# Kernel optimization log

Hardware: AMD Instinct MI355X
Metric: run time of the kernel (lower is better)

The kernel has to match this reference:

```python
import jax, jax.numpy as jnp
import numpy as np

L, N, E, D, H, B = 4, 50000, 800000, 128, 64, 16384
ED = 2 * D  # edge_dim
K = 7      # conv1d kernel size


def setup_inputs() -> dict:
    key = jax.random.key(0)
    ks = jax.random.split(key, 12)
    return {
        "x_nodes": jax.random.normal(ks[0], (L, N, 1), jnp.float32),
        "edge_index": jax.random.randint(ks[1], (L, 2, E), 0, N),
        "W1": jax.random.normal(ks[2], (L, 1, H), jnp.float32) * 0.1,
        "b1": jnp.zeros((L, H), jnp.float32),
        "gamma": jnp.ones((L, H), jnp.float32),
        "beta": jnp.zeros((L, H), jnp.float32),
        "W2": jax.random.normal(ks[3], (L, H, D), jnp.float32) * 0.05,
        "b2": jnp.zeros((L, D), jnp.float32),
        "conv_w": jax.random.normal(ks[4], (ED, ED, K), jnp.float32) * 0.02,
        "conv_b": jnp.zeros((ED,), jnp.float32),
        "lc_w": jax.random.normal(ks[5], (ED, L), jnp.float32) * 0.05,
        "lc_b": jnp.zeros((L,), jnp.float32),
        "link_w": jax.random.normal(ks[6], (ED, 2), jnp.float32) * 0.05,
        "link_b": jnp.zeros((2,), jnp.float32),
        "now_layer": jax.random.randint(ks[7], (B,), 0, L),
        "leftnode": jax.random.randint(ks[8], (B,), 0, N),
        "rightnode": jax.random.randint(ks[9], (B,), 0, N),
    }


def gcn_conv(x, src, dst, norm, W, b):
    # x: [N, Fin] -> [N, Fout]; symmetric-normalized message passing (GCNConv)
    xw = x @ W
    out = jax.ops.segment_sum(norm[:, None] * xw[src], dst, num_segments=N)
    return out + b


def gcn_layer(x, ei, W1, b1, g, bt, W2, b2):
    loops = jnp.arange(N, dtype=ei.dtype)
    src = jnp.concatenate([ei[0], loops])
    dst = jnp.concatenate([ei[1], loops])
    deg = jax.ops.segment_sum(jnp.ones_like(src, jnp.float32), dst, num_segments=N)
    dis = jax.lax.rsqrt(jnp.maximum(deg, 1e-12))
    norm = dis[src] * dis[dst]
    h = gcn_conv(x, src, dst, norm, W1, b1)
    # BatchNorm1d (training mode: batch stats over nodes)
    mu = h.mean(axis=0)
    var = h.var(axis=0)
    h = g * (h - mu) * jax.lax.rsqrt(var + 1e-5) + bt
    h = jax.nn.relu(h)
    return gcn_conv(h, src, dst, norm, W2, b2)


def reference(x_nodes, edge_index, W1, b1, gamma, beta, W2, b2,
              conv_w, conv_b, lc_w, lc_b, link_w, link_b,
              now_layer, leftnode, rightnode):
    # Per-layer GCN embeddings (fixed small L -> Python loop is fine, keeps peak memory low)
    embeds = jnp.stack([
        gcn_layer(x_nodes[i], edge_index[i], W1[i], b1[i], gamma[i], beta[i], W2[i], b2[i])
        for i in range(L)
    ])  # [L, N, D]

    # Edge features: gather per-sample layer-specific node embeddings and concat
    left = embeds[now_layer, leftnode]    # [B, D]
    right = embeds[now_layer, rightnode]  # [B, D]
    layer_specific = jnp.concatenate([left, right], axis=-1)  # [B, ED]

    # Conv1d applied unbatched on [ED, B] (convolves across batch dim, as in original)
    dn = jax.lax.conv_dimension_numbers((1, ED, B), (ED, ED, K), ('NCH', 'OIH', 'NCH'))
    y = jax.lax.conv_general_dilated(layer_specific.T[None], conv_w, (1,), [(3, 3)],
                                     dimension_numbers=dn)[0]  # [ED, B]
    shared = jax.nn.relu(y + conv_b[:, None]).T  # [B, ED]

    discriminant_outs = shared @ lc_w + lc_b  # [B, L]

    # Ortho_algorithm: remove shared component from specific, combine with shared
    dot = jnp.sum(layer_specific * shared, axis=-1, keepdims=True)
    nrm = jnp.sum(shared * shared, axis=-1, keepdims=True)
    enhanced = layer_specific - (dot / (nrm + 1e-12)) * shared + shared  # [B, ED]

    prediction_outs = enhanced @ link_w + link_b  # [B, 2]
    return prediction_outs, discriminant_outs
```

## Files before the change

### kernel.cpp

```cpp
#include <hip/hip_runtime.h>
#include <hip/hip_bf16.h>

#define Lc 4
#define Nc 50000
#define Ec 800000
#define Bc 16384
#define EDc 256
#define Kc 7
#define Mtot (Lc * Nc)
#define NBK 196
#define KDIM (EDc * Kc)

#define BINW 512
#define FB 98
#define NBINS (FB * Lc)
#define CAPc 12288
#define CHUNK 8192

typedef __attribute__((ext_vector_type(8))) short bf16x8;
typedef __attribute__((ext_vector_type(4))) float f32x4;

static __device__ __forceinline__ unsigned short f2bf(float f) {
    unsigned u = __float_as_uint(f);
    unsigned r = (u + 0x7fffu + ((u >> 16) & 1u)) >> 16;
    return (unsigned short)r;
}


__global__ void k_binfill(const int* __restrict__ ei, int* __restrict__ binCursor,
                          int* __restrict__ binned) {
    int l = blockIdx.y;
    int e0 = blockIdx.x * CHUNK;
    __shared__ int lh[FB], lcur[FB];
    if (threadIdx.x < FB) lh[threadIdx.x] = 0;
    __syncthreads();
    const int* srcp = ei + (size_t)l * 2 * Ec;
    const int* dstp = srcp + Ec;
#pragma unroll
    for (int it = 0; it < CHUNK / 256; it++) {
        int idx = e0 + it * 256 + threadIdx.x;
        if (idx < Ec) atomicAdd(&lh[dstp[idx] >> 9], 1);
    }
    __syncthreads();
    if (threadIdx.x < FB) {
        int c = lh[threadIdx.x];
        int bin = l * FB + threadIdx.x;
        int st = c ? atomicAdd(&binCursor[bin], c) : 0;
        lcur[threadIdx.x] = bin * CAPc + min(st, CAPc);
        lh[threadIdx.x] = bin * CAPc + CAPc;
    }
    __syncthreads();
#pragma unroll
    for (int it = 0; it < CHUNK / 256; it++) {
        int idx = e0 + it * 256 + threadIdx.x;
        if (idx < Ec) {
            int d = dstp[idx], sv = srcp[idx];
            int t = d >> 9;
            int pos = atomicAdd(&lcur[t], 1);
            if (pos < lh[t]) binned[pos] = (sv << 9) | (d & (BINW - 1));
        }
    }
}

__global__ __launch_bounds__(512) void k_csr(const int* __restrict__ binCnt,
                                             const int* __restrict__ binned,
                                             int* __restrict__ csr,
                                             int* __restrict__ rstart,
                                             int* __restrict__ cnt,
                                             float* __restrict__ dis) {
    int b = blockIdx.x;
    int l = b / FB, g = b % FB;
    int rs = b * CAPc;
    int cntb = binCnt[b];
    if (cntb > CAPc) cntb = CAPc;
    int re = rs + cntb;
    __shared__ int hist[BINW];
    hist[threadIdx.x] = 0;
    __syncthreads();
    for (int i = rs + threadIdx.x; i < re; i += 512)
        atomicAdd(&hist[binned[i] & (BINW - 1)], 1);
    __syncthreads();
    int lane = threadIdx.x & 63, wid = threadIdx.x >> 6;
    int v = hist[threadIdx.x];
    int x = v;
#pragma unroll
    for (int off = 1; off < 64; off <<= 1) {
        int y = __shfl_up(x, off);
        if (lane >= off) x += y;
    }
    __shared__ int ws[8];
    if (lane == 63) ws[wid] = x;
    __syncthreads();
    int carry = 0;
    for (int w = 0; w < wid; w++) carry += ws[w];
    int exc = x - v + carry;
    int n = g * BINW + threadIdx.x;
    int n4 = l * Nc + n;
    if (n < Nc) {
        rstart[n4] = rs + exc;
        cnt[n4] = v;
        dis[n4] = rsqrtf((float)v + 1.0f);
    }
    __syncthreads();
    hist[threadIdx.x] = rs + exc;
    __syncthreads();
    for (int i = rs + threadIdx.x; i < re; i += 512) {
        unsigned p = (unsigned)binned[i];
        int pos = atomicAdd(&hist[p & (BINW - 1)], 1);
        csr[pos] = (int)(p >> 9);
    }
}


__global__ void k_s_stats4(const int* __restrict__ row_start, const int* __restrict__ cnt,
                           const int* __restrict__ csr, const float* __restrict__ dis,
                           const float* __restrict__ x_nodes, float* __restrict__ s,
                           double* __restrict__ stats) {
    int l = blockIdx.x / NBK;
    int n = (blockIdx.x % NBK) * 256 + threadIdx.x;
    double v = 0.0, v2 = 0.0;
    if (n < Nc) {
        int n4 = l * Nc + n;
        const float* x = x_nodes + (size_t)l * Nc;
        const float* dl = dis + (size_t)l * Nc;
        int st = row_start[n4], en = st + cnt[n4];
        float t = 0.f;
        for (int e = st; e < en; e++) {
            int sv = csr[e];
            t += dl[sv] * x[sv];
        }
        float dn = dl[n];
        float sf = dn * t + dn * dn * x[n];
        s[n4] = sf;
        v = (double)sf;
        v2 = (double)sf * (double)sf;
    }
    for (int m = 32; m; m >>= 1) { v += __shfl_xor(v, m); v2 += __shfl_xor(v2, m); }
    __shared__ double r0[4], r1[4];
    int wid = threadIdx.x >> 6, lane = threadIdx.x & 63;
    if (lane == 0) { r0[wid] = v; r1[wid] = v2; }
    __syncthreads();
    if (threadIdx.x == 0) {
        atomicAdd(&stats[l * 2 + 0], r0[0] + r0[1] + r0[2] + r0[3]);
        atomicAdd(&stats[l * 2 + 1], r1[0] + r1[1] + r1[2] + r1[3]);
    }
}

__global__ void k_cvec4(const double* __restrict__ stats, const float* __restrict__ W1,
                        const float* __restrict__ gamma, float* __restrict__ cbuf) {
    int l = threadIdx.x >> 6, h = threadIdx.x & 63;
    double mean = stats[l * 2] / (double)Nc;
    double var = stats[l * 2 + 1] / (double)Nc - mean * mean;
    float w = W1[l * 64 + h];
    cbuf[l * 72 + h] = gamma[l * 64 + h] * w * rsqrtf((float)var * w * w + 1e-5f);
    if (h == 0) cbuf[l * 72 + 64] = (float)mean;
}


__global__ __launch_bounds__(128) void k_embed4(const int* __restrict__ now,
        const int* __restrict__ lnn, const int* __restrict__ rnn,
        const int* __restrict__ row_start, const int* __restrict__ cnt,
        const int* __restrict__ csr, const float* __restrict__ dis,
        const float* __restrict__ s, const float* __restrict__ cbuf,
        const float* __restrict__ beta, const float* __restrict__ W2,
        const float* __restrict__ b2, float* __restrict__ lsb,
        unsigned short* __restrict__ lsbh) {
    int b = blockIdx.x;
    int l = now[b];
    int side = threadIdx.x >> 6, lane = threadIdx.x & 63;
    int n = side ? rnn[b] : lnn[b];
    int n4 = l * Nc + n;
    float c = cbuf[l * 72 + lane], mu = cbuf[l * 72 + 64], bt = beta[l * 64 + lane];
    const float* dl = dis + (size_t)l * Nc;
    const float* sl = s + (size_t)l * Nc;
    int st = row_start[n4], deg = cnt[n4];
    float a = 0.f;
    for (int base = 0; base < deg; base += 64) {
        int e = base + lane;
        int sv = (e < deg) ? csr[st + e] : 0;
        float nv = (e < deg) ? dl[sv] : 0.f;
        float fv = (e < deg) ? sl[sv] : 0.f;
        int m = min(64, deg - base);
        for (int j = 0; j < m; j++) {
            float nj = __shfl(nv, j);
            float fj = __shfl(fv, j);
            float hv = fmaxf(c * (fj - mu) + bt, 0.f);
            a += nj * hv;
        }
    }
    float dn = dl[n];
    float hself = fmaxf(c * (sl[n] - mu) + bt, 0.f);
    a = dn * a + dn * dn * hself;
    const float* W2l = W2 + (size_t)l * 64 * 128;
    const float* b2l = b2 + (size_t)l * 128;
    float o0 = b2l[lane], o1 = b2l[lane + 64];
    for (int hh = 0; hh < 64; hh++) {
        float ah = __shfl(a, hh);
        o0 += ah * W2l[hh * 128 + lane];
        o1 += ah * W2l[hh * 128 + lane + 64];
    }
    size_t obase = (size_t)b * 256 + side * 128;
    lsb[obase + lane] = o0;
    lsb[obase + lane + 64] = o1;
    lsbh[obase + lane] = f2bf(o0);
    lsbh[obase + lane + 64] = f2bf(o1);
}


__global__ void k_wbf(const float* __restrict__ w, unsigned short* __restrict__ wbt) {
    int i = blockIdx.x * 256 + threadIdx.x;
    int co = i / KDIM;
    int r = i % KDIM;
    int ci = r / Kc, k = r % Kc;
    wbt[(size_t)co * KDIM + k * EDc + ci] = f2bf(w[i]);
}

__global__ __launch_bounds__(512, 1) void k_convmma(const unsigned short* __restrict__ lsbh,
                                                    const unsigned short* __restrict__ wbt,
                                                    const float* __restrict__ cb,
                                                    float* __restrict__ sh) {
    __shared__ unsigned short lsa[70 * EDc];
    int b0 = blockIdx.x * 64;
    int wid = threadIdx.x >> 6, lane = threadIdx.x & 63;
    int lrow = lane & 15, lg = lane >> 4;

    for (int idx = threadIdx.x; idx < 70 * 32; idx += 512) {
        int r = idx >> 5, c = idx & 31;
        int grow = b0 - 3 + r;
        uint4 v = make_uint4(0u, 0u, 0u, 0u);
        if ((unsigned)grow < (unsigned)Bc)
            v = *(const uint4*)(lsbh + (size_t)grow * EDc + c * 8);
        int byte = (r * 512 + c * 16) ^ ((r & 7) << 4);
        *(uint4*)((char*)lsa + byte) = v;
    }
    __syncthreads();

    const unsigned short* w0 = wbt + (size_t)(wid * 32 + lrow) * KDIM + lg * 8;

    f32x4 acc[4][2] = {};
    bf16x8 br0[8][2], br1[8][2];

#pragma unroll
    for (int tt = 0; tt < 8; tt++)
#pragma unroll
        for (int ni = 0; ni < 2; ni++)
            br0[tt][ni] = *(const bf16x8*)(w0 + ni * 16 * KDIM + tt * 32);

#pragma unroll
    for (int k = 0; k < Kc; k++) {
        if (k < Kc - 1) {
#pragma unroll
            for (int tt = 0; tt < 8; tt++)
#pragma unroll
                for (int ni = 0; ni < 2; ni++) {
                    bf16x8 v = *(const bf16x8*)(w0 + ni * 16 * KDIM + (k + 1) * 256 + tt * 32);
                    if (k & 1) br0[tt][ni] = v; else br1[tt][ni] = v;
                }
        }
#pragma unroll
        for (int tt = 0; tt < 8; tt++) {
            bf16x8 a[4];
#pragma unroll
            for (int mi = 0; mi < 4; mi++) {
                int l = mi * 16 + lrow + k;
                a[mi] = *(const bf16x8*)((const char*)lsa + l * 512
                        + ((lg * 16 + tt * 64) ^ ((l & 7) << 4)));
            }
#pragma unroll
            for (int mi = 0; mi < 4; mi++)
#pragma unroll
                for (int ni = 0; ni < 2; ni++) {
                    bf16x8 bv = (k & 1) ? br1[tt][ni] : br0[tt][ni];
                    acc[mi][ni] = __builtin_amdgcn_mfma_f32_16x16x32_bf16(
                        a[mi], bv, acc[mi][ni], 0, 0, 0);
                }
        }
    }

#pragma unroll
    for (int mi = 0; mi < 4; mi++) {
        int rbase = b0 + mi * 16 + lg * 4;
#pragma unroll
        for (int ni = 0; ni < 2; ni++) {
            int co = wid * 32 + ni * 16 + lrow;
            float bias = cb[co];
#pragma unroll
            for (int r = 0; r < 4; r++)
                sh[(size_t)(rbase + r) * EDc + co] = fmaxf(acc[mi][ni][r] + bias, 0.0f);
        }
    }
}

__global__ void k_final(const float* __restrict__ ls, const float* __restrict__ sh,
                        const float* __restrict__ lc_w, const float* __restrict__ lc_b,
                        const float* __restrict__ link_w, const float* __restrict__ link_b,
                        float* __restrict__ out) {
    int b = blockIdx.x, lane = threadIdx.x;
    float lsv[4], shv[4];
    float dot = 0.f, nrm = 0.f;
#pragma unroll
    for (int i = 0; i < 4; i++) {
        int ci = lane + i * 64;
        lsv[i] = ls[b * 256 + ci];
        shv[i] = sh[b * 256 + ci];
        dot += lsv[i] * shv[i];
        nrm += shv[i] * shv[i];
    }
    for (int m = 32; m; m >>= 1) { dot += __shfl_xor(dot, m); nrm += __shfl_xor(nrm, m); }
    float coef = dot / (nrm + 1e-12f);
    float p0 = 0.f, p1 = 0.f, d0 = 0.f, d1 = 0.f, d2 = 0.f, d3 = 0.f;
#pragma unroll
    for (int i = 0; i < 4; i++) {
        int ci = lane + i * 64;
        float e = lsv[i] - coef * shv[i] + shv[i];
        p0 += e * link_w[ci * 2];
        p1 += e * link_w[ci * 2 + 1];
        d0 += shv[i] * lc_w[ci * 4];
        d1 += shv[i] * lc_w[ci * 4 + 1];
        d2 += shv[i] * lc_w[ci * 4 + 2];
        d3 += shv[i] * lc_w[ci * 4 + 3];
    }
    for (int m = 32; m; m >>= 1) {
        p0 += __shfl_xor(p0, m); p1 += __shfl_xor(p1, m);
        d0 += __shfl_xor(d0, m); d1 += __shfl_xor(d1, m);
        d2 += __shfl_xor(d2, m); d3 += __shfl_xor(d3, m);
    }
    if (lane == 0) {
        out[b * 2]     = p0 + link_b[0];
        out[b * 2 + 1] = p1 + link_b[1];
        float* dd = out + 2 * Bc;
        dd[b * 4]     = d0 + lc_b[0];
        dd[b * 4 + 1] = d1 + lc_b[1];
        dd[b * 4 + 2] = d2 + lc_b[2];
        dd[b * 4 + 3] = d3 + lc_b[3];
    }
}


extern "C" void kernel_launch(void* const* d_in, const int* in_sizes, int n_in,
                              void* d_out, int out_size, void* d_ws, size_t ws_size,
                              hipStream_t stream) {
    const float* x_nodes    = (const float*)d_in[0];
    const int*   edge_index = (const int*)d_in[1];
    const float* W1   = (const float*)d_in[2];
    const float* gamma = (const float*)d_in[4];
    const float* beta  = (const float*)d_in[5];
    const float* W2   = (const float*)d_in[6];
    const float* b2   = (const float*)d_in[7];
    const float* conv_w = (const float*)d_in[8];
    const float* conv_b = (const float*)d_in[9];
    const float* lc_w   = (const float*)d_in[10];
    const float* lc_b   = (const float*)d_in[11];
    const float* link_w = (const float*)d_in[12];
    const float* link_b = (const float*)d_in[13];
    const int* now = (const int*)d_in[14];
    const int* ln  = (const int*)d_in[15];
    const int* rn  = (const int*)d_in[16];
    float* out = (float*)d_out;

    char* base = (char*)d_ws;
    size_t off = 0;
    auto carve = [&](size_t bytes) {
        void* p = base + off;
        off = (off + bytes + 255) & ~(size_t)255;
        return p;
    };
    int*    binCursor = (int*)carve(NBINS * 4);
    double* stats     = (double*)carve(8 * 8);
    int*    binned    = (int*)carve((size_t)NBINS * CAPc * 4);
    int*    rstart    = (int*)carve((size_t)Mtot * 4);
    int*    cnt       = (int*)carve((size_t)Mtot * 4);
    int*    csr       = (int*)carve((size_t)NBINS * CAPc * 4);
    float*  dis       = (float*)carve((size_t)Mtot * 4);
    float*  s         = (float*)carve((size_t)Mtot * 4);
    float*  cbuf      = (float*)carve(Lc * 72 * 4);
    float*  lsb       = (float*)carve((size_t)Bc * 256 * 4);
    float*  shb       = (float*)carve((size_t)Bc * 256 * 4);
    unsigned short* lsbh = (unsigned short*)carve((size_t)Bc * 256 * 2);
    unsigned short* wbt  = (unsigned short*)carve((size_t)EDc * KDIM * 2);
    (void)ws_size;

    const int FBLK = (Ec + CHUNK - 1) / CHUNK;

    hipMemsetAsync(binCursor, 0, (char*)(stats + 8) - (char*)binCursor, stream);
    k_wbf<<<1792, 256, 0, stream>>>(conv_w, wbt);

    k_binfill<<<dim3(FBLK, Lc), 256, 0, stream>>>(edge_index, binCursor, binned);
    k_csr<<<NBINS, 512, 0, stream>>>(binCursor, binned, csr, rstart, cnt, dis);
    k_s_stats4<<<NBK * Lc, 256, 0, stream>>>(rstart, cnt, csr, dis, x_nodes, s, stats);
    k_cvec4<<<1, 256, 0, stream>>>(stats, W1, gamma, cbuf);
    k_embed4<<<Bc, 128, 0, stream>>>(now, ln, rn, rstart, cnt, csr, dis, s,
                                     cbuf, beta, W2, b2, lsb, lsbh);

    k_convmma<<<Bc / 64, 512, 0, stream>>>(lsbh, wbt, conv_b, shb);
    k_final<<<Bc, 64, 0, stream>>>(lsb, shb, lc_w, lc_b, link_w, link_b, out);
}
```

Baseline: 210.1 us.

## Compute first-layer aggregation from binned edges with shared-memory atomics

The first GCN aggregation (s = D^-1/2 A D^-1/2 x) now runs directly over the coarse binned edge lists, one block per 512-node bin, accumulating into shared-memory floats with atomics instead of walking per-node CSR rows. The CSR kernel additionally precomputes g = dis*x per node, so each edge needs only one gather. This replaces the divergent per-thread row loops with coalesced streaming over bins. In exchange, float atomic accumulation order becomes nondeterministic, and an extra Mtot-sized buffer is written and read.

```diff
diff --git a/kernel.cpp b/kernel.cpp
--- a/kernel.cpp
+++ b/kernel.cpp
@@ -8,7 +8,6 @@
 #define EDc 256
 #define Kc 7
 #define Mtot (Lc * Nc)
-#define NBK 196
 #define KDIM (EDc * Kc)
 
 #define BINW 512
@@ -64,12 +63,14 @@
 
 __global__ __launch_bounds__(512) void k_csr(const int* __restrict__ binCnt,
                                              const int* __restrict__ binned,
+                                             const float* __restrict__ x_nodes,
                                              int* __restrict__ csr,
                                              int* __restrict__ rstart,
                                              int* __restrict__ cnt,
-                                             float* __restrict__ dis) {
+                                             float* __restrict__ dis,
+                                             float* __restrict__ g) {
     int b = blockIdx.x;
-    int l = b / FB, g = b % FB;
+    int l = b / FB, gg = b % FB;
     int rs = b * CAPc;
     int cntb = binCnt[b];
     if (cntb > CAPc) cntb = CAPc;
@@ -94,12 +95,14 @@
     int carry = 0;
     for (int w = 0; w < wid; w++) carry += ws[w];
     int exc = x - v + carry;
-    int n = g * BINW + threadIdx.x;
+    int n = gg * BINW + threadIdx.x;
     int n4 = l * Nc + n;
     if (n < Nc) {
         rstart[n4] = rs + exc;
         cnt[n4] = v;
-        dis[n4] = rsqrtf((float)v + 1.0f);
+        float dn = rsqrtf((float)v + 1.0f);
+        dis[n4] = dn;
+        g[n4] = dn * x_nodes[(size_t)l * Nc + n];
     }
     __syncthreads();
     hist[threadIdx.x] = rs + exc;
@@ -112,37 +115,47 @@
 }
 
 
-__global__ void k_s_stats4(const int* __restrict__ row_start, const int* __restrict__ cnt,
-                           const int* __restrict__ csr, const float* __restrict__ dis,
-                           const float* __restrict__ x_nodes, float* __restrict__ s,
-                           double* __restrict__ stats) {
-    int l = blockIdx.x / NBK;
-    int n = (blockIdx.x % NBK) * 256 + threadIdx.x;
+__global__ __launch_bounds__(512) void k_s_bin(const int* __restrict__ binCnt,
+                                               const int* __restrict__ binned,
+                                               const float* __restrict__ g,
+                                               const float* __restrict__ dis,
+                                               float* __restrict__ s,
+                                               double* __restrict__ stats) {
+    int b = blockIdx.x;
+    int l = b / FB, gg = b % FB;
+    int rs = b * CAPc;
+    int cntb = binCnt[b];
+    if (cntb > CAPc) cntb = CAPc;
+    int re = rs + cntb;
+    const float* gl = g + (size_t)l * Nc;
+    __shared__ float acc[BINW];
+    acc[threadIdx.x] = 0.f;
+    __syncthreads();
+    for (int i = rs + threadIdx.x; i < re; i += 512) {
+        unsigned p = (unsigned)binned[i];
+        atomicAdd(&acc[p & (BINW - 1)], gl[p >> 9]);
+    }
+    __syncthreads();
+    int n = gg * BINW + threadIdx.x;
+    int n4 = l * Nc + n;
     double v = 0.0, v2 = 0.0;
     if (n < Nc) {
-        int n4 = l * Nc + n;
-        const float* x = x_nodes + (size_t)l * Nc;
-        const float* dl = dis + (size_t)l * Nc;
-        int st = row_start[n4], en = st + cnt[n4];
-        float t = 0.f;
-        for (int e = st; e < en; e++) {
-            int sv = csr[e];
-            t += dl[sv] * x[sv];
-        }
-        float dn = dl[n];
-        float sf = dn * t + dn * dn * x[n];
+        float dn = dis[n4];
+        float sf = dn * (acc[threadIdx.x] + g[n4]);
         s[n4] = sf;
         v = (double)sf;
         v2 = (double)sf * (double)sf;
     }
     for (int m = 32; m; m >>= 1) { v += __shfl_xor(v, m); v2 += __shfl_xor(v2, m); }
-    __shared__ double r0[4], r1[4];
+    __shared__ double r0[8], r1[8];
     int wid = threadIdx.x >> 6, lane = threadIdx.x & 63;
     if (lane == 0) { r0[wid] = v; r1[wid] = v2; }
     __syncthreads();
     if (threadIdx.x == 0) {
-        atomicAdd(&stats[l * 2 + 0], r0[0] + r0[1] + r0[2] + r0[3]);
-        atomicAdd(&stats[l * 2 + 1], r1[0] + r1[1] + r1[2] + r1[3]);
+        double a = 0, bb = 0;
+        for (int w = 0; w < 8; w++) { a += r0[w]; bb += r1[w]; }
+        atomicAdd(&stats[l * 2 + 0], a);
+        atomicAdd(&stats[l * 2 + 1], bb);
     }
 }
 
@@ -373,6 +386,7 @@
     int*    csr       = (int*)carve((size_t)NBINS * CAPc * 4);
     float*  dis       = (float*)carve((size_t)Mtot * 4);
     float*  s         = (float*)carve((size_t)Mtot * 4);
+    float*  g         = (float*)carve((size_t)Mtot * 4);
     float*  cbuf      = (float*)carve(Lc * 72 * 4);
     float*  lsb       = (float*)carve((size_t)Bc * 256 * 4);
     float*  shb       = (float*)carve((size_t)Bc * 256 * 4);
@@ -386,8 +400,8 @@
     k_wbf<<<1792, 256, 0, stream>>>(conv_w, wbt);
 
     k_binfill<<<dim3(FBLK, Lc), 256, 0, stream>>>(edge_index, binCursor, binned);
-    k_csr<<<NBINS, 512, 0, stream>>>(binCursor, binned, csr, rstart, cnt, dis);
-    k_s_stats4<<<NBK * Lc, 256, 0, stream>>>(rstart, cnt, csr, dis, x_nodes, s, stats);
+    k_csr<<<NBINS, 512, 0, stream>>>(binCursor, binned, x_nodes, csr, rstart, cnt, dis, g);
+    k_s_bin<<<NBINS, 512, 0, stream>>>(binCursor, binned, g, dis, s, stats);
     k_cvec4<<<1, 256, 0, stream>>>(stats, W1, gamma, cbuf);
     k_embed4<<<Bc, 128, 0, stream>>>(now, ln, rn, rstart, cnt, csr, dis, s,
                                      cbuf, beta, W2, b2, lsb, lsbh);
```

Result: faster. 185.3 us (-11.8%).
